# Optimization experiments

Measured on AMD Instinct MI355X. Metric: run time of the kernel, lower is better.

## Reference

```python
import jax, jax.numpy as jnp
import numpy as np

CLASSES = [20, 70, 250, 800, 3000, 12000]
DIM = 768
B = 2048


def setup_inputs() -> dict:
    key = jax.random.key(0)
    ks = jax.random.split(key, 2 * len(CLASSES) + 1)
    inp = {"x": jax.random.normal(ks[0], (B, DIM), jnp.float32)}
    scale = 1.0 / np.sqrt(DIM).astype(np.float32)
    for i, c in enumerate(CLASSES):
        # Concatenation of all per-node generator Linear layers at level i.
        inp[f"W{i}"] = jax.random.normal(ks[1 + i], (c, DIM), jnp.float32) * scale
        inp[f"b{i}"] = jnp.zeros((c,), jnp.float32)
    for lvl in range(1, 6):
        k = jax.random.fold_in(key, 100 + lvl)
        # parent index (at level lvl-1) of each class at level lvl; sorted -> contiguous sibling groups
        inp[f"p{lvl}"] = jnp.sort(
            jax.random.randint(k, (CLASSES[lvl],), 0, CLASSES[lvl - 1], jnp.int32)
        )
    return inp


def _segment_softmax_cols(logits, parent, num_parents):
    """Softmax over columns of logits [B, C], within groups of columns sharing a parent."""
    lt = logits.T  # [C, B]
    mx = jax.ops.segment_max(lt, parent, num_segments=num_parents)  # [P, B]
    e = jnp.exp(lt - mx[parent])
    s = jax.ops.segment_sum(e, parent, num_segments=num_parents)  # [P, B]
    return (e / s[parent]).T  # [B, C]


def reference(x, W0, b0, W1, b1, W2, b2, W3, b3, W4, b4, W5, b5, p1, p2, p3, p4, p5):
    # Level 0: root generator = Linear + Softmax over all level-0 classes.
    out = jax.nn.softmax(x @ W0.T + b0, axis=1)  # [B, classes[0]]
    outputs = [out]
    Ws = [W1, W2, W3, W4, W5]
    bs = [b1, b2, b3, b4, b5]
    ps = [p1, p2, p3, p4, p5]
    for lvl in range(5):
        logits = x @ Ws[lvl].T + bs[lvl]  # [B, classes[lvl+1]]
        cond = _segment_softmax_cols(logits, ps[lvl], CLASSES[lvl])  # per-parent softmax
        out = cond * outputs[-1][:, ps[lvl]]  # scatter of prob * subtree(x) == gather of parent prob
        outputs.append(out)
    return tuple(outputs)
```

## Files before the change

### kernel.cpp

```cpp
#include <hip/hip_runtime.h>
#include <stdint.h>

#define BDIM 2048
#define KDIM 768
#define NTOT 16140
#define NKT 24

typedef _Float16 half8 __attribute__((ext_vector_type(8)));
typedef float floatx4 __attribute__((ext_vector_type(4)));

__device__ __forceinline__ unsigned short f2h(float f) {
  _Float16 h = (_Float16)f;
  return __builtin_bit_cast(unsigned short, h);
}

__device__ __forceinline__ void level_of(int col, int& cb, int& Cl, long long& ob) {
  if      (col < 20)   { cb = 0;    Cl = 20;    ob = 0LL; }
  else if (col < 90)   { cb = 20;   Cl = 70;    ob = 40960LL; }
  else if (col < 340)  { cb = 90;   Cl = 250;   ob = 184320LL; }
  else if (col < 1140) { cb = 340;  Cl = 800;   ob = 696320LL; }
  else if (col < 4140) { cb = 1140; Cl = 3000;  ob = 2334720LL; }
  else                 { cb = 4140; Cl = 12000; ob = 8478720LL; }
}

__device__ __forceinline__ void gload_lds16(const void* g, void* l) {
  __builtin_amdgcn_global_load_lds(
      (const __attribute__((address_space(1))) unsigned int*)g,
      (__attribute__((address_space(3))) unsigned int*)l, 16, 0, 0);
}

#define PREP_STR 524288LL
#define CONV_N   3492096LL

__device__ __forceinline__ void conv_addr(
    long long i4, const float* x,
    const float* W0, const float* W1, const float* W2,
    const float* W3, const float* W4, const float* W5,
    unsigned short* xh, unsigned short* wh,
    const float4*& s, ushort4*& d)
{
  long long e = i4 * 4;
  const long long XN = (long long)BDIM * KDIM;
  if (e < XN) {
    s = reinterpret_cast<const float4*>(x) + i4;
    d = reinterpret_cast<ushort4*>(xh + e);
  } else {
    long long we = e - XN;
    const float* src; long long off;
    if      (we < 15360)    { src = W0; off = we; }
    else if (we < 69120)    { src = W1; off = we - 15360; }
    else if (we < 261120)   { src = W2; off = we - 69120; }
    else if (we < 875520)   { src = W3; off = we - 261120; }
    else if (we < 3179520)  { src = W4; off = we - 875520; }
    else                    { src = W5; off = we - 3179520; }
    s = reinterpret_cast<const float4*>(src) + (off >> 2);
    d = reinterpret_cast<ushort4*>(wh + we);
  }
}

__device__ __forceinline__ ushort4 cvt4(float4 v) {
  ushort4 o;
  o.x = f2h(v.x); o.y = f2h(v.y); o.z = f2h(v.z); o.w = f2h(v.w);
  return o;
}

__global__ __launch_bounds__(256) void prep_kernel(
    const float* __restrict__ x,
    const float* __restrict__ W0, const float* __restrict__ W1,
    const float* __restrict__ W2, const float* __restrict__ W3,
    const float* __restrict__ W4, const float* __restrict__ W5,
    const float* __restrict__ b0, const float* __restrict__ b1, const float* __restrict__ b2,
    const float* __restrict__ b3, const float* __restrict__ b4, const float* __restrict__ b5,
    const int* __restrict__ p1, const int* __restrict__ p2, const int* __restrict__ p3,
    const int* __restrict__ p4, const int* __restrict__ p5,
    unsigned short* __restrict__ xh, unsigned short* __restrict__ wh,
    int* __restrict__ gst, float* __restrict__ bcat)
{
  const long long gtid = (long long)blockIdx.x * 256 + threadIdx.x;

  if (gtid < 4142) {
    int j = (int)gtid;
    int val;
    if (j == 0) val = 0;
    else if (j == 4141) val = 16140;
    else {
      const int* p; int C, s, base;
      if      (j < 21)   { p = p1; C = 70;    s = j - 1;    base = 20; }
      else if (j < 91)   { p = p2; C = 250;   s = j - 21;   base = 90; }
      else if (j < 341)  { p = p3; C = 800;   s = j - 91;   base = 340; }
      else if (j < 1141) { p = p4; C = 3000;  s = j - 341;  base = 1140; }
      else               { p = p5; C = 12000; s = j - 1141; base = 4140; }
      int lo = 0, hi = C;
      while (lo < hi) { int mid = (lo + hi) >> 1; if (p[mid] < s) lo = mid + 1; else hi = mid; }
      val = base + lo;
    }
    gst[j] = val;
  } else if (gtid < 4142 + 16140) {
    int col = (int)(gtid - 4142);
    int cb, Cl; long long ob; level_of(col, cb, Cl, ob);
    const float* bs;
    if      (col < 20)   bs = b0;
    else if (col < 90)   bs = b1;
    else if (col < 340)  bs = b2;
    else if (col < 1140) bs = b3;
    else if (col < 4140) bs = b4;
    else                 bs = b5;
    bcat[col] = bs[col - cb];
  }

  long long i = gtid;
  while (i + PREP_STR < CONV_N) {
    const float4 *s0, *s1; ushort4 *d0, *d1;
    conv_addr(i,            x, W0, W1, W2, W3, W4, W5, xh, wh, s0, d0);
    conv_addr(i + PREP_STR, x, W0, W1, W2, W3, W4, W5, xh, wh, s1, d1);
    float4 a = *s0;
    float4 b = *s1;
    *d0 = cvt4(a);
    *d1 = cvt4(b);
    i += 2 * PREP_STR;
  }
  if (i < CONV_N) {
    const float4* s0; ushort4* d0;
    conv_addr(i, x, W0, W1, W2, W3, W4, W5, xh, wh, s0, d0);
    *d0 = cvt4(*s0);
  }
}

#define EPI_STRIDE 132

__global__ __launch_bounds__(256, 2) void gemm_kernel(
    const unsigned short* __restrict__ Ah,
    const unsigned short* __restrict__ Wh,
    float* __restrict__ out)
{
  __shared__ __align__(16) char smem_raw[64 * EPI_STRIDE * 4];
  float* epi = (float*)smem_raw;

  const int bid = blockIdx.x;
  const int logical = (bid & 7) * 254 + (bid >> 3);
  const int cx = logical >> 4;
  const int row0 = (logical & 15) * 128;
  const int col0 = cx * 128;

  const int tid  = threadIdx.x;
  const int wave = tid >> 6;
  const int lane = tid & 63;
  const int wr = (wave >> 1) * 64;
  const int wc = (wave & 1) * 64;
  const int q  = lane >> 4;
  const int lr = lane & 15;

  const int rquad = lane >> 2;
  const int kq = lane & 3;

  floatx4 acc[4][4];
#pragma unroll
  for (int i = 0; i < 4; ++i)
#pragma unroll
    for (int j = 0; j < 4; ++j)
      acc[i][j] = (floatx4){0.f, 0.f, 0.f, 0.f};

  const unsigned short* gA[2];
  const unsigned short* gB[2];
#pragma unroll
  for (int i = 0; i < 2; ++i) {
    int c = 2 * wave + i;
    int rowA = row0 + 16 * c + rquad;
    gA[i] = Ah + (long long)rowA * KDIM + kq * 8;
    int colB = col0 + 16 * c + rquad;
    if (colB >= NTOT) colB = NTOT - 1;
    gB[i] = Wh + (long long)colB * KDIM + kq * 8;
  }

  auto stage = [&](int buf, int kt) {
#pragma unroll
    for (int i = 0; i < 2; ++i) {
      int c = 2 * wave + i;
      gload_lds16(gA[i] + kt * 32, smem_raw + buf * 8192 + c * 1024);
      gload_lds16(gB[i] + kt * 32, smem_raw + 16384 + buf * 8192 + c * 1024);
    }
  };

  int cur = 0;
  stage(0, 0);
  __syncthreads();

  for (int kt = 0; kt < NKT; ++kt) {
    if (kt + 1 < NKT) stage(cur ^ 1, kt + 1);
    const char* Ac = smem_raw + cur * 8192;
    const char* Bc = smem_raw + 16384 + cur * 8192;
    half8 af[4], bf[4];
#pragma unroll
    for (int i = 0; i < 4; ++i)
      af[i] = __builtin_bit_cast(half8, *(const uint4*)(Ac + (wr + i * 16 + lr) * 64 + q * 16));
#pragma unroll
    for (int j = 0; j < 4; ++j)
      bf[j] = __builtin_bit_cast(half8, *(const uint4*)(Bc + (wc + j * 16 + lr) * 64 + q * 16));
#pragma unroll
    for (int i = 0; i < 4; ++i)
#pragma unroll
      for (int j = 0; j < 4; ++j)
        acc[i][j] = __builtin_amdgcn_mfma_f32_16x16x32_f16(af[i], bf[j], acc[i][j], 0, 0, 0);
    __syncthreads();
    cur ^= 1;
  }

  int cbA, ClA; long long obA; level_of(col0, cbA, ClA, obA);
  int cbB, ClB; long long obB; level_of(col0 + 127, cbB, ClB, obB);
  const bool fast = (cbA == cbB) && ((cbA & 3) == 0) && ((ClA & 3) == 0) && (col0 + 128 <= NTOT);

  for (int h = 0; h < 2; ++h) {
    __syncthreads();
    if ((wave >> 1) == h) {
#pragma unroll
      for (int i = 0; i < 4; ++i)
#pragma unroll
        for (int j = 0; j < 4; ++j)
#pragma unroll
          for (int rg = 0; rg < 4; ++rg)
            epi[(i * 16 + q * 4 + rg) * EPI_STRIDE + wc + j * 16 + lr] = acc[i][j][rg];
    }
    __syncthreads();
    if (fast) {
      const long long rowbase = obA + (long long)(row0 + h * 64) * ClA + (col0 - cbA);
#pragma unroll
      for (int it = 0; it < 8; ++it) {
        int idx = it * 256 + tid;
        int r = idx >> 5, f4 = idx & 31;
        float4 v = *(const float4*)(epi + r * EPI_STRIDE + f4 * 4);
        *(float4*)(out + rowbase + (long long)r * ClA + f4 * 4) = v;
      }
    } else {
      for (int idx = tid; idx < 64 * 128; idx += 256) {
        int r = idx >> 7, c = idx & 127;
        int col = col0 + c;
        if (col < NTOT) {
          int cb, Cl; long long ob; level_of(col, cb, Cl, ob);
          out[ob + (long long)(row0 + h * 64 + r) * Cl + (col - cb)] = epi[r * EPI_STRIDE + c];
        }
      }
    }
  }
}

__global__ __launch_bounds__(1024) void tree_softmax_kernel(
    float* __restrict__ out,
    const float* __restrict__ bcat, const int* __restrict__ gst,
    const int* __restrict__ p1, const int* __restrict__ p2, const int* __restrict__ p3,
    const int* __restrict__ p4, const int* __restrict__ p5)
{
  __shared__ __align__(16) float l[NTOT];
  __shared__ __align__(16) float S[4141];
  const int tid = threadIdx.x;
  const long long row = blockIdx.x;

  if (tid < 340) {
    float v;
    if      (tid < 20) v = out[row * 20 + tid] + bcat[tid];
    else if (tid < 90) v = out[40960 + row * 70 + (tid - 20)] + bcat[tid];
    else               v = out[184320 + row * 250 + (tid - 90)] + bcat[tid];
    l[tid] = __expf(v);
  }
  if (tid < 200) {
    float4 v = reinterpret_cast<const float4*>(out + 696320 + row * 800)[tid];
    float4 b = reinterpret_cast<const float4*>(bcat + 340)[tid];
    float4 e;
    e.x = __expf(v.x + b.x); e.y = __expf(v.y + b.y);
    e.z = __expf(v.z + b.z); e.w = __expf(v.w + b.w);
    reinterpret_cast<float4*>(l + 340)[tid] = e;
  }
  if (tid < 750) {
    float4 v = reinterpret_cast<const float4*>(out + 2334720 + row * 3000)[tid];
    float4 b = reinterpret_cast<const float4*>(bcat + 1140)[tid];
    float4 e;
    e.x = __expf(v.x + b.x); e.y = __expf(v.y + b.y);
    e.z = __expf(v.z + b.z); e.w = __expf(v.w + b.w);
    reinterpret_cast<float4*>(l + 1140)[tid] = e;
  }
  for (int i4 = tid; i4 < 3000; i4 += 1024) {
    float4 v = reinterpret_cast<const float4*>(out + 8478720 + row * 12000)[i4];
    float4 b = reinterpret_cast<const float4*>(bcat + 4140)[i4];
    float4 e;
    e.x = __expf(v.x + b.x); e.y = __expf(v.y + b.y);
    e.z = __expf(v.z + b.z); e.w = __expf(v.w + b.w);
    reinterpret_cast<float4*>(l + 4140)[i4] = e;
  }
  __syncthreads();

  for (int j = tid; j < 4141; j += 1024) {
    int a = gst[j], b = gst[j + 1];
    float s = 0.f;
    for (int c = a; c < b; ++c) s += l[c];
    S[j] = s;
  }
  __syncthreads();

  if (tid < 20) {
    float s0 = S[0];
    float inv = 1.f / s0;
    float t = l[tid] * inv / S[1 + tid];
    S[1 + tid] = t;
    if (tid == 0) S[0] = inv;
  }
  __syncthreads();
  if (tid < 70)
    S[21 + tid] = l[20 + tid] * S[1 + p1[tid]] / S[21 + tid];
  __syncthreads();
  if (tid < 250)
    S[91 + tid] = l[90 + tid] * S[21 + p2[tid]] / S[91 + tid];
  __syncthreads();
  if (tid < 800)
    S[341 + tid] = l[340 + tid] * S[91 + p3[tid]] / S[341 + tid];
  __syncthreads();
  for (int s = tid; s < 3000; s += 1024)
    S[1141 + s] = l[1140 + s] * S[341 + p4[s]] / S[1141 + s];
  __syncthreads();

  if (tid < 340) {
    if (tid < 20)      out[row * 20 + tid] = l[tid] * S[0];
    else if (tid < 90) out[40960 + row * 70 + (tid - 20)] = l[tid] * S[1 + p1[tid - 20]];
    else               out[184320 + row * 250 + (tid - 90)] = l[tid] * S[21 + p2[tid - 90]];
  }
  if (tid < 200) {
    int4 p = reinterpret_cast<const int4*>(p3)[tid];
    float4 e = reinterpret_cast<const float4*>(l + 340)[tid];
    e.x *= S[91 + p.x]; e.y *= S[91 + p.y]; e.z *= S[91 + p.z]; e.w *= S[91 + p.w];
    reinterpret_cast<float4*>(out + 696320 + row * 800)[tid] = e;
  }
  if (tid < 750) {
    int4 p = reinterpret_cast<const int4*>(p4)[tid];
    float4 e = reinterpret_cast<const float4*>(l + 1140)[tid];
    e.x *= S[341 + p.x]; e.y *= S[341 + p.y]; e.z *= S[341 + p.z]; e.w *= S[341 + p.w];
    reinterpret_cast<float4*>(out + 2334720 + row * 3000)[tid] = e;
  }
  for (int i4 = tid; i4 < 3000; i4 += 1024) {
    int4 p = reinterpret_cast<const int4*>(p5)[i4];
    float4 e = reinterpret_cast<const float4*>(l + 4140)[i4];
    e.x *= S[1141 + p.x]; e.y *= S[1141 + p.y]; e.z *= S[1141 + p.z]; e.w *= S[1141 + p.w];
    reinterpret_cast<float4*>(out + 8478720 + row * 12000)[i4] = e;
  }
}

extern "C" void kernel_launch(void* const* d_in, const int* in_sizes, int n_in,
                              void* d_out, int out_size, void* d_ws, size_t ws_size,
                              hipStream_t stream)
{
  const float* x = (const float*)d_in[0];
  const float* W[6]    = {(const float*)d_in[1], (const float*)d_in[3], (const float*)d_in[5],
                          (const float*)d_in[7], (const float*)d_in[9], (const float*)d_in[11]};
  const float* bias[6] = {(const float*)d_in[2], (const float*)d_in[4], (const float*)d_in[6],
                          (const float*)d_in[8], (const float*)d_in[10], (const float*)d_in[12]};
  const int* p[5] = {(const int*)d_in[13], (const int*)d_in[14], (const int*)d_in[15],
                     (const int*)d_in[16], (const int*)d_in[17]};
  float* out = (float*)d_out;
  char* ws = (char*)d_ws;
  unsigned short* xh = (unsigned short*)ws;
  unsigned short* wh = (unsigned short*)(ws + 3145728);
  int* gst = (int*)(ws + 27936768);
  float* bcat = (float*)(ws + 27953344);

  prep_kernel<<<2048, 256, 0, stream>>>(
      x, W[0], W[1], W[2], W[3], W[4], W[5],
      bias[0], bias[1], bias[2], bias[3], bias[4], bias[5],
      p[0], p[1], p[2], p[3], p[4], xh, wh, gst, bcat);
  gemm_kernel<<<2032, 256, 0, stream>>>(xh, wh, out);
  tree_softmax_kernel<<<2048, 1024, 0, stream>>>(
      out, bcat, gst, p[0], p[1], p[2], p[3], p[4]);
}
```

Baseline: 338.2 us.

## Fuse fp32-to-fp16 weight conversion into GEMM B-tile loading

The prep kernel no longer converts the weight matrices to fp16 in a workspace. The GEMM instead loads fp32 weights straight from the per-level inputs into registers, converts them, and writes them to LDS with a two-stage register prefetch. This removes a full read and write pass over about 12M weight elements. In exchange the GEMM reads twice as many bytes for B, since each weight tile is reread by the 16 row blocks, and it uses more registers and VALU work per tile.

New measurement: 354.6 us. 4.8% more time.

```diff
diff --git a/kernel.cpp b/kernel.cpp
--- a/kernel.cpp
+++ b/kernel.cpp
@@ -29,57 +29,25 @@
       (__attribute__((address_space(3))) unsigned int*)l, 16, 0, 0);
 }
 
-#define PREP_STR 524288LL
-#define CONV_N   3492096LL
-
-__device__ __forceinline__ void conv_addr(
-    long long i4, const float* x,
-    const float* W0, const float* W1, const float* W2,
-    const float* W3, const float* W4, const float* W5,
-    unsigned short* xh, unsigned short* wh,
-    const float4*& s, ushort4*& d)
-{
-  long long e = i4 * 4;
-  const long long XN = (long long)BDIM * KDIM;
-  if (e < XN) {
-    s = reinterpret_cast<const float4*>(x) + i4;
-    d = reinterpret_cast<ushort4*>(xh + e);
-  } else {
-    long long we = e - XN;
-    const float* src; long long off;
-    if      (we < 15360)    { src = W0; off = we; }
-    else if (we < 69120)    { src = W1; off = we - 15360; }
-    else if (we < 261120)   { src = W2; off = we - 69120; }
-    else if (we < 875520)   { src = W3; off = we - 261120; }
-    else if (we < 3179520)  { src = W4; off = we - 875520; }
-    else                    { src = W5; off = we - 3179520; }
-    s = reinterpret_cast<const float4*>(src) + (off >> 2);
-    d = reinterpret_cast<ushort4*>(wh + we);
-  }
-}
-
-__device__ __forceinline__ ushort4 cvt4(float4 v) {
-  ushort4 o;
-  o.x = f2h(v.x); o.y = f2h(v.y); o.z = f2h(v.z); o.w = f2h(v.w);
-  return o;
-}
-
 __global__ __launch_bounds__(256) void prep_kernel(
     const float* __restrict__ x,
-    const float* __restrict__ W0, const float* __restrict__ W1,
-    const float* __restrict__ W2, const float* __restrict__ W3,
-    const float* __restrict__ W4, const float* __restrict__ W5,
     const float* __restrict__ b0, const float* __restrict__ b1, const float* __restrict__ b2,
     const float* __restrict__ b3, const float* __restrict__ b4, const float* __restrict__ b5,
     const int* __restrict__ p1, const int* __restrict__ p2, const int* __restrict__ p3,
     const int* __restrict__ p4, const int* __restrict__ p5,
-    unsigned short* __restrict__ xh, unsigned short* __restrict__ wh,
-    int* __restrict__ gst, float* __restrict__ bcat)
+    unsigned short* __restrict__ xh, int* __restrict__ gst, float* __restrict__ bcat)
 {
-  const long long gtid = (long long)blockIdx.x * 256 + threadIdx.x;
-
-  if (gtid < 4142) {
-    int j = (int)gtid;
+  long long gtid = (long long)blockIdx.x * 256 + threadIdx.x;
+  if (gtid < 393216LL) {
+    float4 v = reinterpret_cast<const float4*>(x)[gtid];
+    ushort4 o;
+    o.x = f2h(v.x); o.y = f2h(v.y); o.z = f2h(v.z); o.w = f2h(v.w);
+    reinterpret_cast<ushort4*>(xh)[gtid] = o;
+    return;
+  }
+  long long u = gtid - 393216LL;
+  if (u < 4142) {
+    int j = (int)u;
     int val;
     if (j == 0) val = 0;
     else if (j == 4141) val = 16140;
@@ -95,8 +63,11 @@
       val = base + lo;
     }
     gst[j] = val;
-  } else if (gtid < 4142 + 16140) {
-    int col = (int)(gtid - 4142);
+    return;
+  }
+  long long v5 = u - 4142;
+  if (v5 < 16140) {
+    int col = (int)v5;
     int cb, Cl; long long ob; level_of(col, cb, Cl, ob);
     const float* bs;
     if      (col < 20)   bs = b0;
@@ -107,30 +78,15 @@
     else                 bs = b5;
     bcat[col] = bs[col - cb];
   }
-
-  long long i = gtid;
-  while (i + PREP_STR < CONV_N) {
-    const float4 *s0, *s1; ushort4 *d0, *d1;
-    conv_addr(i,            x, W0, W1, W2, W3, W4, W5, xh, wh, s0, d0);
-    conv_addr(i + PREP_STR, x, W0, W1, W2, W3, W4, W5, xh, wh, s1, d1);
-    float4 a = *s0;
-    float4 b = *s1;
-    *d0 = cvt4(a);
-    *d1 = cvt4(b);
-    i += 2 * PREP_STR;
-  }
-  if (i < CONV_N) {
-    const float4* s0; ushort4* d0;
-    conv_addr(i, x, W0, W1, W2, W3, W4, W5, xh, wh, s0, d0);
-    *d0 = cvt4(*s0);
-  }
 }
 
 #define EPI_STRIDE 132
 
 __global__ __launch_bounds__(256, 2) void gemm_kernel(
     const unsigned short* __restrict__ Ah,
-    const unsigned short* __restrict__ Wh,
+    const float* __restrict__ Wf0, const float* __restrict__ Wf1,
+    const float* __restrict__ Wf2, const float* __restrict__ Wf3,
+    const float* __restrict__ Wf4, const float* __restrict__ Wf5,
     float* __restrict__ out)
 {
   __shared__ __align__(16) char smem_raw[64 * EPI_STRIDE * 4];
@@ -161,32 +117,72 @@
       acc[i][j] = (floatx4){0.f, 0.f, 0.f, 0.f};
 
   const unsigned short* gA[2];
-  const unsigned short* gB[2];
 #pragma unroll
   for (int i = 0; i < 2; ++i) {
     int c = 2 * wave + i;
     int rowA = row0 + 16 * c + rquad;
     gA[i] = Ah + (long long)rowA * KDIM + kq * 8;
-    int colB = col0 + 16 * c + rquad;
-    if (colB >= NTOT) colB = NTOT - 1;
-    gB[i] = Wh + (long long)colB * KDIM + kq * 8;
-  }
-
-  auto stage = [&](int buf, int kt) {
+  }
+  auto stageA = [&](int buf, int kt) {
 #pragma unroll
     for (int i = 0; i < 2; ++i) {
       int c = 2 * wave + i;
       gload_lds16(gA[i] + kt * 32, smem_raw + buf * 8192 + c * 1024);
-      gload_lds16(gB[i] + kt * 32, smem_raw + 16384 + buf * 8192 + c * 1024);
     }
   };
 
+  const float* gBs[2];
+#pragma unroll
+  for (int i = 0; i < 2; ++i) {
+    int s = tid + i * 256;
+    int colB = col0 + (s >> 2);
+    if (colB >= NTOT) colB = NTOT - 1;
+    int cb, Cl; long long ob; level_of(colB, cb, Cl, ob);
+    const float* Wp;
+    if      (colB < 20)   Wp = Wf0;
+    else if (colB < 90)   Wp = Wf1;
+    else if (colB < 340)  Wp = Wf2;
+    else if (colB < 1140) Wp = Wf3;
+    else if (colB < 4140) Wp = Wf4;
+    else                  Wp = Wf5;
+    gBs[i] = Wp + (long long)(colB - cb) * KDIM + (s & 3) * 8;
+  }
+
+  float4 rb[2][2];
+  auto loadB = [&](int kt) {
+    const int kb = kt * 32;
+#pragma unroll
+    for (int i = 0; i < 2; ++i) {
+      rb[i][0] = *reinterpret_cast<const float4*>(gBs[i] + kb);
+      rb[i][1] = *reinterpret_cast<const float4*>(gBs[i] + kb + 4);
+    }
+  };
+  auto writeB = [&](int buf) {
+#pragma unroll
+    for (int i = 0; i < 2; ++i) {
+      int s = tid + i * 256;
+      union { ushort u[8]; uint4 v; } pk;
+      pk.u[0] = f2h(rb[i][0].x); pk.u[1] = f2h(rb[i][0].y);
+      pk.u[2] = f2h(rb[i][0].z); pk.u[3] = f2h(rb[i][0].w);
+      pk.u[4] = f2h(rb[i][1].x); pk.u[5] = f2h(rb[i][1].y);
+      pk.u[6] = f2h(rb[i][1].z); pk.u[7] = f2h(rb[i][1].w);
+      *reinterpret_cast<uint4*>(smem_raw + 16384 + buf * 8192 + s * 16) = pk.v;
+    }
+  };
+
+  stageA(0, 0);
+  loadB(0);
+  writeB(0);
+  loadB(1);
+  __syncthreads();
+
   int cur = 0;
-  stage(0, 0);
-  __syncthreads();
-
   for (int kt = 0; kt < NKT; ++kt) {
-    if (kt + 1 < NKT) stage(cur ^ 1, kt + 1);
+    if (kt + 1 < NKT) {
+      stageA(cur ^ 1, kt + 1);
+      writeB(cur ^ 1);
+    }
+    if (kt + 2 < NKT) loadB(kt + 2);
     const char* Ac = smem_raw + cur * 8192;
     const char* Bc = smem_raw + 16384 + cur * 8192;
     half8 af[4], bf[4];
@@ -355,15 +351,14 @@
   float* out = (float*)d_out;
   char* ws = (char*)d_ws;
   unsigned short* xh = (unsigned short*)ws;
-  unsigned short* wh = (unsigned short*)(ws + 3145728);
   int* gst = (int*)(ws + 27936768);
   float* bcat = (float*)(ws + 27953344);
 
-  prep_kernel<<<2048, 256, 0, stream>>>(
-      x, W[0], W[1], W[2], W[3], W[4], W[5],
-      bias[0], bias[1], bias[2], bias[3], bias[4], bias[5],
-      p[0], p[1], p[2], p[3], p[4], xh, wh, gst, bcat);
-  gemm_kernel<<<2032, 256, 0, stream>>>(xh, wh, out);
+  prep_kernel<<<1616, 256, 0, stream>>>(
+      x, bias[0], bias[1], bias[2], bias[3], bias[4], bias[5],
+      p[0], p[1], p[2], p[3], p[4], xh, gst, bcat);
+  gemm_kernel<<<2032, 256, 0, stream>>>(
+      xh, W[0], W[1], W[2], W[3], W[4], W[5], out);
   tree_softmax_kernel<<<2048, 1024, 0, stream>>>(
       out, bcat, gst, p[0], p[1], p[2], p[3], p[4]);
 }
```
